# Optimization experiments

Hardware: AMD Instinct MI355X
Metric: run time of the kernel (lower is better)

Reference implementation:

```python
import jax, jax.numpy as jnp
import numpy as np

NUM_CLASSES = 6

def _weight_matrix(num_classes, weight_type='quadratic'):
    i = jnp.arange(num_classes, dtype=jnp.float32)
    d = jnp.abs(i[:, None] - i[None, :])
    if weight_type == 'linear':
        return d
    elif weight_type == 'quadratic':
        return d ** 2
    else:
        raise ValueError("weight_type must be 'linear' or 'quadratic'")

def setup_inputs() -> dict:
    key = jax.random.key(0)
    k1, k2 = jax.random.split(key)
    N = 4_000_000
    y_pred = jax.random.normal(k1, (N, NUM_CLASSES), dtype=jnp.float32)
    y_true = jax.random.randint(k2, (N,), 0, NUM_CLASSES, dtype=jnp.int64)
    return {"y_pred": y_pred, "y_true": y_true}

def reference(y_pred, y_true):
    C = NUM_CLASSES
    t = y_true.reshape(-1).astype(jnp.int32)
    probs = jax.nn.softmax(y_pred, axis=1)
    p = jnp.argmax(probs, axis=1).astype(jnp.int32)
    # histograms over classes (equivalent to torch.histc with bins=C, min=0, max=C-1)
    hist_true = jnp.bincount(t, length=C).astype(jnp.float32)
    hist_pred = jnp.bincount(p, length=C).astype(jnp.float32)
    # confusion matrix in one fused scatter-add pass (replaces the Python loop)
    flat = t * C + p  # [N]
    confusion = jnp.bincount(flat, length=C * C).astype(jnp.float32).reshape(C, C)
    confusion = confusion / confusion.sum()
    expected = jnp.outer(hist_true, hist_pred)
    expected = expected / expected.sum()
    W = _weight_matrix(C, 'quadratic')
    kappa = 1.0 - (W * confusion).sum() / (W * expected).sum()
    return kappa
```

## Files before the change

### kernel.cpp

```cpp
#include <hip/hip_runtime.h>


#define NC 6
#define NBINS 36
#define BLOCK 1024
#define NWAVES (BLOCK / 64)
#define GRID 512
#define CHUNK 64
#define SEGS 16
#define FIN_THREADS (NBINS * SEGS)

__global__ __launch_bounds__(BLOCK, 8) void kappa_count(
    const float4* __restrict__ yp4, const int2* __restrict__ yt2,
    const float* __restrict__ yp, const int* __restrict__ yt,
    unsigned int* __restrict__ gconf, int npairs, int N) {
    __shared__ float4 stage[NWAVES][3 * CHUNK];
    __shared__ unsigned int sconf[NWAVES][NBINS];
    const int tid = threadIdx.x;
    const int w = tid >> 6;
    const int L = tid & 63;
    if (tid < NWAVES * NBINS) ((unsigned int*)sconf)[tid] = 0u;
    __syncthreads();

    unsigned int* my = sconf[w];
    float4* st = stage[w];

    const int nchunks = npairs / CHUNK;
    const int gwaves = GRID * NWAVES;
    for (int c = blockIdx.x * NWAVES + w; c < nchunks; c += gwaves) {
        const float4 g0 = yp4[c * 3 * CHUNK + L];
        const float4 g1 = yp4[c * 3 * CHUNK + 64 + L];
        const float4 g2 = yp4[c * 3 * CHUNK + 128 + L];
        const int2 t = yt2[c * CHUNK + L];
        st[L] = g0;
        st[64 + L] = g1;
        st[128 + L] = g2;
        __threadfence_block();
        const float4 a = st[3 * L];
        const float4 b = st[3 * L + 1];
        const float4 d = st[3 * L + 2];

        float m = a.x; int p = 0;
        if (a.y > m) { m = a.y; p = 1; }
        if (a.z > m) { m = a.z; p = 2; }
        if (a.w > m) { m = a.w; p = 3; }
        if (b.x > m) { m = b.x; p = 4; }
        if (b.y > m) { m = b.y; p = 5; }
        atomicAdd(&my[t.x * NC + p], 1u);

        m = b.z; p = 0;
        if (b.w > m) { m = b.w; p = 1; }
        if (d.x > m) { m = d.x; p = 2; }
        if (d.y > m) { m = d.y; p = 3; }
        if (d.z > m) { m = d.z; p = 4; }
        if (d.w > m) { m = d.w; p = 5; }
        atomicAdd(&my[t.y * NC + p], 1u);
    }

    const int rem0 = nchunks * CHUNK;
    if (blockIdx.x == 0 && tid < npairs - rem0) {
        const int i = rem0 + tid;
        const float4 a = yp4[3 * i];
        const float4 b = yp4[3 * i + 1];
        const float4 d = yp4[3 * i + 2];
        const int2 t = yt2[i];
        float m = a.x; int p = 0;
        if (a.y > m) { m = a.y; p = 1; }
        if (a.z > m) { m = a.z; p = 2; }
        if (a.w > m) { m = a.w; p = 3; }
        if (b.x > m) { m = b.x; p = 4; }
        if (b.y > m) { m = b.y; p = 5; }
        atomicAdd(&my[t.x * NC + p], 1u);
        m = b.z; p = 0;
        if (b.w > m) { m = b.w; p = 1; }
        if (d.x > m) { m = d.x; p = 2; }
        if (d.y > m) { m = d.y; p = 3; }
        if (d.z > m) { m = d.z; p = 4; }
        if (d.w > m) { m = d.w; p = 5; }
        atomicAdd(&my[t.y * NC + p], 1u);
    }

    if ((N & 1) && blockIdx.x == 0 && tid == 0) {
        const int r = N - 1;
        float m = yp[r * NC]; int p = 0;
        #pragma unroll
        for (int j = 1; j < NC; ++j) {
            const float v = yp[r * NC + j];
            if (v > m) { m = v; p = j; }
        }
        atomicAdd(&my[yt[r] * NC + p], 1u);
    }

    __syncthreads();
    if (tid < NBINS) {
        unsigned int s = 0;
        #pragma unroll
        for (int k = 0; k < NWAVES; ++k) s += sconf[k][tid];
        gconf[blockIdx.x * NBINS + tid] = s;
    }
}

__global__ void kappa_final_kernel(const unsigned int* __restrict__ gconf,
                                   float* __restrict__ out, long long N) {
    __shared__ unsigned int part[SEGS][NBINS];
    __shared__ unsigned int conf_s[NBINS];
    const int tid = threadIdx.x;
    if (tid < FIN_THREADS) {
        const int bin = tid % NBINS;
        const int seg = tid / NBINS;
        unsigned int s = 0;
        const int b0 = seg * (GRID / SEGS);
        #pragma unroll 8
        for (int b = b0; b < b0 + GRID / SEGS; ++b) s += gconf[b * NBINS + bin];
        part[seg][bin] = s;
    }
    __syncthreads();
    if (tid < NBINS) {
        unsigned int tot = 0;
        #pragma unroll
        for (int s2 = 0; s2 < SEGS; ++s2) tot += part[s2][tid];
        conf_s[tid] = tot;
    }
    __syncthreads();
    if (tid == 0) {
        long long conf[NBINS], ht[NC], hp[NC];
        #pragma unroll
        for (int i = 0; i < NC; ++i) { ht[i] = 0; hp[i] = 0; }
        #pragma unroll
        for (int k = 0; k < NBINS; ++k) conf[k] = (long long)conf_s[k];

        long long num = 0;
        #pragma unroll
        for (int i = 0; i < NC; ++i)
            #pragma unroll
            for (int j = 0; j < NC; ++j) {
                const long long w = (long long)(i - j) * (i - j);
                num += w * conf[i * NC + j];
                ht[i] += conf[i * NC + j];
                hp[j] += conf[i * NC + j];
            }
        long long den = 0;
        #pragma unroll
        for (int i = 0; i < NC; ++i)
            #pragma unroll
            for (int j = 0; j < NC; ++j)
                den += (long long)(i - j) * (i - j) * ht[i] * hp[j];

        out[0] = (float)(1.0 - ((double)num * (double)N) / (double)den);
    }
}

extern "C" void kernel_launch(void* const* d_in, const int* in_sizes, int n_in,
                              void* d_out, int out_size, void* d_ws, size_t ws_size,
                              hipStream_t stream) {
    const float* yp = (const float*)d_in[0];
    const int* yt = (const int*)d_in[1];
    const int N = in_sizes[1];
    unsigned int* gconf = (unsigned int*)d_ws;

    const int npairs = N / 2;
    kappa_count<<<GRID, BLOCK, 0, stream>>>(
        (const float4*)yp, (const int2*)yt, yp, yt, gconf, npairs, N);
    kappa_final_kernel<<<1, FIN_THREADS, 0, stream>>>(gconf, (float*)d_out,
                                                      (long long)N);
}
```

Baseline: 155.6 us.

## Load rows directly into registers with 4-way unrolled batches, smaller blocks

Drops the shared-memory staging of each wave's float4 chunk. Each lane now loads its own pair of rows straight from global memory with strided float4 loads. Each wave processes 256 pairs per iteration, with four independent load groups issued before the compare-and-count work to raise memory-level parallelism. Block size drops to 256 and the grid grows to 2048. The per-lane strided loads are less coalesced than the earlier staged layout, which could cost bandwidth.

```diff
diff --git a/kernel.cpp b/kernel.cpp
--- a/kernel.cpp
+++ b/kernel.cpp
@@ -3,81 +3,83 @@
 
 #define NC 6
 #define NBINS 36
-#define BLOCK 1024
-#define NWAVES (BLOCK / 64)
-#define GRID 512
-#define CHUNK 64
+#define BLOCK 256
+#define WPB (BLOCK / 64)
+#define PAIRS_PER_WAVE 256
+#define GRID 2048
 #define SEGS 16
 #define FIN_THREADS (NBINS * SEGS)
 
-__global__ __launch_bounds__(BLOCK, 8) void kappa_count(
+__global__ __launch_bounds__(BLOCK) void kappa_count(
     const float4* __restrict__ yp4, const int2* __restrict__ yt2,
     const float* __restrict__ yp, const int* __restrict__ yt,
     unsigned int* __restrict__ gconf, int npairs, int N) {
-    __shared__ float4 stage[NWAVES][3 * CHUNK];
-    __shared__ unsigned int sconf[NWAVES][NBINS];
+    __shared__ unsigned int sconf[WPB][NBINS];
     const int tid = threadIdx.x;
     const int w = tid >> 6;
     const int L = tid & 63;
-    if (tid < NWAVES * NBINS) ((unsigned int*)sconf)[tid] = 0u;
+    if (tid < WPB * NBINS) ((unsigned int*)sconf)[tid] = 0u;
     __syncthreads();
 
     unsigned int* my = sconf[w];
-    float4* st = stage[w];
+    const long long gstride = (long long)GRID * WPB * PAIRS_PER_WAVE;
 
-    const int nchunks = npairs / CHUNK;
-    const int gwaves = GRID * NWAVES;
-    for (int c = blockIdx.x * NWAVES + w; c < nchunks; c += gwaves) {
-        const float4 g0 = yp4[c * 3 * CHUNK + L];
-        const float4 g1 = yp4[c * 3 * CHUNK + 64 + L];
-        const float4 g2 = yp4[c * 3 * CHUNK + 128 + L];
-        const int2 t = yt2[c * CHUNK + L];
-        st[L] = g0;
-        st[64 + L] = g1;
-        st[128 + L] = g2;
-        __threadfence_block();
-        const float4 a = st[3 * L];
-        const float4 b = st[3 * L + 1];
-        const float4 d = st[3 * L + 2];
-
-        float m = a.x; int p = 0;
-        if (a.y > m) { m = a.y; p = 1; }
-        if (a.z > m) { m = a.z; p = 2; }
-        if (a.w > m) { m = a.w; p = 3; }
-        if (b.x > m) { m = b.x; p = 4; }
-        if (b.y > m) { m = b.y; p = 5; }
-        atomicAdd(&my[t.x * NC + p], 1u);
-
-        m = b.z; p = 0;
-        if (b.w > m) { m = b.w; p = 1; }
-        if (d.x > m) { m = d.x; p = 2; }
-        if (d.y > m) { m = d.y; p = 3; }
-        if (d.z > m) { m = d.z; p = 4; }
-        if (d.w > m) { m = d.w; p = 5; }
-        atomicAdd(&my[t.y * NC + p], 1u);
-    }
-
-    const int rem0 = nchunks * CHUNK;
-    if (blockIdx.x == 0 && tid < npairs - rem0) {
-        const int i = rem0 + tid;
-        const float4 a = yp4[3 * i];
-        const float4 b = yp4[3 * i + 1];
-        const float4 d = yp4[3 * i + 2];
-        const int2 t = yt2[i];
-        float m = a.x; int p = 0;
-        if (a.y > m) { m = a.y; p = 1; }
-        if (a.z > m) { m = a.z; p = 2; }
-        if (a.w > m) { m = a.w; p = 3; }
-        if (b.x > m) { m = b.x; p = 4; }
-        if (b.y > m) { m = b.y; p = 5; }
-        atomicAdd(&my[t.x * NC + p], 1u);
-        m = b.z; p = 0;
-        if (b.w > m) { m = b.w; p = 1; }
-        if (d.x > m) { m = d.x; p = 2; }
-        if (d.y > m) { m = d.y; p = 3; }
-        if (d.z > m) { m = d.z; p = 4; }
-        if (d.w > m) { m = d.w; p = 5; }
-        atomicAdd(&my[t.y * NC + p], 1u);
+    for (long long base = ((long long)blockIdx.x * WPB + w) * PAIRS_PER_WAVE;
+         base < npairs; base += gstride) {
+        if (base + PAIRS_PER_WAVE <= npairs) {
+            float4 A[4], B[4], D[4];
+            int2 T[4];
+            #pragma unroll
+            for (int k = 0; k < 4; ++k) {
+                const long long i = base + (long long)k * 64 + L;
+                A[k] = yp4[3 * i];
+                B[k] = yp4[3 * i + 1];
+                D[k] = yp4[3 * i + 2];
+                T[k] = yt2[i];
+            }
+            #pragma unroll
+            for (int k = 0; k < 4; ++k) {
+                float m = A[k].x; int p = 0;
+                if (A[k].y > m) { m = A[k].y; p = 1; }
+                if (A[k].z > m) { m = A[k].z; p = 2; }
+                if (A[k].w > m) { m = A[k].w; p = 3; }
+                if (B[k].x > m) { m = B[k].x; p = 4; }
+                if (B[k].y > m) { m = B[k].y; p = 5; }
+                atomicAdd(&my[T[k].x * NC + p], 1u);
+                m = B[k].z; p = 0;
+                if (B[k].w > m) { m = B[k].w; p = 1; }
+                if (D[k].x > m) { m = D[k].x; p = 2; }
+                if (D[k].y > m) { m = D[k].y; p = 3; }
+                if (D[k].z > m) { m = D[k].z; p = 4; }
+                if (D[k].w > m) { m = D[k].w; p = 5; }
+                atomicAdd(&my[T[k].y * NC + p], 1u);
+            }
+        } else {
+            #pragma unroll
+            for (int k = 0; k < 4; ++k) {
+                const long long i = base + (long long)k * 64 + L;
+                if (i < npairs) {
+                    const float4 a = yp4[3 * i];
+                    const float4 b = yp4[3 * i + 1];
+                    const float4 d = yp4[3 * i + 2];
+                    const int2 t = yt2[i];
+                    float m = a.x; int p = 0;
+                    if (a.y > m) { m = a.y; p = 1; }
+                    if (a.z > m) { m = a.z; p = 2; }
+                    if (a.w > m) { m = a.w; p = 3; }
+                    if (b.x > m) { m = b.x; p = 4; }
+                    if (b.y > m) { m = b.y; p = 5; }
+                    atomicAdd(&my[t.x * NC + p], 1u);
+                    m = b.z; p = 0;
+                    if (b.w > m) { m = b.w; p = 1; }
+                    if (d.x > m) { m = d.x; p = 2; }
+                    if (d.y > m) { m = d.y; p = 3; }
+                    if (d.z > m) { m = d.z; p = 4; }
+                    if (d.w > m) { m = d.w; p = 5; }
+                    atomicAdd(&my[t.y * NC + p], 1u);
+                }
+            }
+        }
     }
 
     if ((N & 1) && blockIdx.x == 0 && tid == 0) {
@@ -95,7 +97,7 @@
     if (tid < NBINS) {
         unsigned int s = 0;
         #pragma unroll
-        for (int k = 0; k < NWAVES; ++k) s += sconf[k][tid];
+        for (int k = 0; k < WPB; ++k) s += sconf[k][tid];
         gconf[blockIdx.x * NBINS + tid] = s;
     }
 }
```

New measurement: 157.5 us. Within noise of the previous version (+1.2%).
